# Performance work log

Measured on AMD Instinct MI355X. Metric: run time of the kernel, lower is better.

## Reference

```python
import jax, jax.numpy as jnp
import numpy as np

B, S, D = 4, 4096, 1024  # batch, seq_len, input_dim == key_dim == value_dim == output_dim


def setup_inputs() -> dict:
    key = jax.random.key(0)
    kx, kq, kk, kv, kp = jax.random.split(key, 5)
    scale = 1.0 / np.sqrt(D)
    return {
        "x": jax.random.normal(kx, (B, S, D), dtype=jnp.float32),
        # weights stored as (in_dim, out_dim) so projection is x @ W
        "Wq": jax.random.normal(kq, (D, D), dtype=jnp.float32) * scale,
        "Wk": jax.random.normal(kk, (D, D), dtype=jnp.float32) * scale,
        "Wv": jax.random.normal(kv, (D, D), dtype=jnp.float32) * scale,
        "P": jax.random.normal(kp, (D, D), dtype=jnp.float32) * scale,
    }


def reference(x, Wq, Wk, Wv, P):
    # Linear (softmax-free) self-attention, faithful to the torch module:
    # Q K^T then (.)V, materializing the (B,S,S) score matrix as the original does.
    Q = jnp.einsum("bsd,dk->bsk", x, Wq)
    K = jnp.einsum("bsd,dk->bsk", x, Wk)
    V = jnp.einsum("bsd,dv->bsv", x, Wv)
    scores = jnp.einsum("bsk,btk->bst", Q, K)   # (B,S,S)
    context = jnp.einsum("bst,btv->bsv", scores, V)
    return x + jnp.einsum("bsv,vo->bso", context, P)
```

## Files before the change

### kernel.cpp

```cpp
#include <hip/hip_runtime.h>
#include <hip/hip_bf16.h>
#include <stdint.h>


#define BATCH 4
#define SEQ   4096
#define DIM   1024

#define TRI_SLICE 589824l

typedef __bf16 bf16x8 __attribute__((ext_vector_type(8)));
typedef float f32x4 __attribute__((ext_vector_type(4)));

static __device__ __forceinline__ unsigned short f2bf(float f) {
    unsigned int u = __builtin_bit_cast(unsigned int, f);
    u += 0x7fff + ((u >> 16) & 1);
    return (unsigned short)(u >> 16);
}
static __device__ __forceinline__ float bf2f(unsigned short h) {
    unsigned int u = (unsigned int)h << 16;
    return __builtin_bit_cast(float, u);
}

__global__ __launch_bounds__(256)
void gemm_fin(const unsigned short* __restrict__ Ag,
              const unsigned short* __restrict__ Btg,
              float* __restrict__ Cg,
              int K, int lda, int ldbt, int ldc,
              long sA, long sBt, long sC)
{
    __shared__ unsigned short As[3][128][32];
    __shared__ unsigned short Bs[3][256][32];

    const int gx = gridDim.x, gy = gridDim.y;
    const int nwg = gx * gy * gridDim.z;
    int id = blockIdx.x + gx * (blockIdx.y + gy * blockIdx.z);
    id = (id & 7) * (nwg >> 3) + (id >> 3);

    const int bx = id % gx;
    const int rest = id / gx;
    const int by = rest % gy;
    const int b = rest / gy;
    const long i0 = (long)by * 128;
    const long j0 = (long)bx * 256;

    const unsigned short* A  = Ag  + (long)b * sA;
    const unsigned short* Bt = Btg + (long)b * sBt;

    const int tid  = threadIdx.x;
    const int lane = tid & 63;
    const int w    = tid >> 6;
    const int wr   = w >> 1, wc = w & 1;
    const int srow = lane >> 2;
    const int sch  = lane & 3;
    const int fr   = lane & 15;
    const int kg   = lane >> 4;
    const int ch   = (kg ^ ((fr >> 1) & 3)) * 8;

    f32x4 acc[4][8] = {};
    const int nt = K / 32;

    auto stage = [&](int t, int buf) {
        const long kk = (long)t * 32;
        const long scoff = (long)((sch ^ ((srow >> 1) & 3)) * 8);
#pragma unroll
        for (int inst = 0; inst < 2; ++inst) {
            const int row = inst * 64 + w * 16 + srow;
            const unsigned short* src = A + (i0 + row) * lda + kk + scoff;
            __builtin_amdgcn_global_load_lds(
                (const __attribute__((address_space(1))) void*)src,
                (__attribute__((address_space(3))) void*)&As[buf][inst * 64 + w * 16][0],
                16, 0, 0);
        }
#pragma unroll
        for (int inst = 0; inst < 4; ++inst) {
            const int row = inst * 64 + w * 16 + srow;
            const unsigned short* src = Bt + (j0 + row) * ldbt + kk + scoff;
            __builtin_amdgcn_global_load_lds(
                (const __attribute__((address_space(1))) void*)src,
                (__attribute__((address_space(3))) void*)&Bs[buf][inst * 64 + w * 16][0],
                16, 0, 0);
        }
    };

    stage(0, 0);
    stage(1, 1);
    stage(2, 2);

    for (int t = 0; t < nt; ++t) {
        const int buf = t % 3;
        if (t < nt - 2)      asm volatile("s_waitcnt vmcnt(12)" ::: "memory");
        else if (t == nt - 2) asm volatile("s_waitcnt vmcnt(6)" ::: "memory");
        else                 asm volatile("s_waitcnt vmcnt(0)" ::: "memory");
        __builtin_amdgcn_s_barrier();
        asm volatile("" ::: "memory");

        bf16x8 af[4], bfv[8];
#pragma unroll
        for (int m = 0; m < 4; ++m)
            af[m] = *(const bf16x8*)&As[buf][wr * 64 + m * 16 + fr][ch];
#pragma unroll
        for (int n = 0; n < 8; ++n)
            bfv[n] = *(const bf16x8*)&Bs[buf][wc * 128 + n * 16 + fr][ch];

        asm volatile("s_waitcnt lgkmcnt(0)" ::: "memory");
        __builtin_amdgcn_sched_barrier(0);
        __builtin_amdgcn_s_barrier();
        asm volatile("" ::: "memory");

        if (t + 3 < nt) stage(t + 3, buf);
        __builtin_amdgcn_sched_barrier(0);

        __builtin_amdgcn_s_setprio(1);
#pragma unroll
        for (int m = 0; m < 4; ++m)
#pragma unroll
            for (int n = 0; n < 8; ++n)
                acc[m][n] = __builtin_amdgcn_mfma_f32_16x16x32_bf16(
                    af[m], bfv[n], acc[m][n], 0, 0, 0);
        __builtin_amdgcn_s_setprio(0);
    }

    float* C32 = Cg + (long)b * sC;
#pragma unroll
    for (int m = 0; m < 4; ++m) {
        const long rbase = i0 + wr * 64 + m * 16 + kg * 4;
#pragma unroll
        for (int n = 0; n < 8; ++n) {
            const long col = j0 + wc * 128 + n * 16 + fr;
#pragma unroll
            for (int q = 0; q < 4; ++q)
                C32[(rbase + q) * ldc + col] = acc[m][n][q];
        }
    }
}

template<int OUTMODE, int BN, bool TRI, bool ADD_I>
__global__ __launch_bounds__(256)
void gemm_db(const unsigned short* __restrict__ Ag,
             const unsigned short* __restrict__ Btg,
             void* __restrict__ Cg,
             int K, int zdiv, int lda, int ldbt, int ldc,
             long sA, long sBt, long sC)
{
    constexpr int NF = BN / 32;
    __shared__ unsigned short As[2][128][64];
    __shared__ unsigned short Bs[2][BN][64];

    const int gx = gridDim.x, gy = gridDim.y;
    const int nwg = gx * gy * gridDim.z;
    int id = blockIdx.x + gx * (blockIdx.y + gy * blockIdx.z);
    id = (id & 7) * (nwg >> 3) + (id >> 3);

    int z, tlin = 0;
    long i0, j0;
    if (TRI) {
        z = id / 36;
        tlin = id % 36;
        int t = tlin, ti = 0;
        while (t > ti) { t -= ti + 1; ++ti; }
        i0 = (long)ti * 128;
        j0 = (long)t * 128;
    } else {
        const int bx = id % gx;
        const int rest = id / gx;
        const int by = rest % gy;
        z = rest / gy;
        i0 = (long)by * 128;
        j0 = (long)bx * BN;
    }
    const int b = z / zdiv;
    const long koff = (long)(z % zdiv) * K;

    const unsigned short* A  = Ag  + (long)b * sA  + koff;
    const unsigned short* Bt = Btg + (long)b * sBt + koff;

    const int tid  = threadIdx.x;
    const int lane = tid & 63;
    const int w    = tid >> 6;
    const int wr   = w >> 1, wc = w & 1;
    const int lrow = lane >> 3;
    const int lcol = lane & 7;
    const int fr   = lane & 15;
    const int kg   = lane >> 4;
    const int scol = (lcol ^ lrow) * 8;

    f32x4 acc[4][NF] = {};

    const int nt = K / 64;

    auto stage = [&](int t, int buf) {
        const long kk = (long)t * 64;
#pragma unroll
        for (int inst = 0; inst < 4; ++inst) {
            const int row = w * 32 + inst * 8;
            const unsigned short* srcA = A + (i0 + row + lrow) * lda + kk + scol;
            __builtin_amdgcn_global_load_lds(
                (const __attribute__((address_space(1))) void*)srcA,
                (__attribute__((address_space(3))) void*)&As[buf][row][0], 16, 0, 0);
        }
#pragma unroll
        for (int inst = 0; inst < NF; ++inst) {
            const int row = w * (8 * NF) + inst * 8;
            const unsigned short* srcB = Bt + (j0 + row + lrow) * ldbt + kk + scol;
            __builtin_amdgcn_global_load_lds(
                (const __attribute__((address_space(1))) void*)srcB,
                (__attribute__((address_space(3))) void*)&Bs[buf][row][0], 16, 0, 0);
        }
    };

    stage(0, 0);
    stage(1, 1);

    for (int t = 0; t < nt; ++t) {
        const int buf = t & 1;
        if (t < nt - 1) {
            if constexpr (BN == 128)
                asm volatile("s_waitcnt vmcnt(8)" ::: "memory");
            else
                asm volatile("s_waitcnt vmcnt(6)" ::: "memory");
        } else {
            asm volatile("s_waitcnt vmcnt(0)" ::: "memory");
        }
        __builtin_amdgcn_s_barrier();
        asm volatile("" ::: "memory");

        bf16x8 af0[4], bf0[NF], af1[4], bf1[NF];
        const int ch0 = (kg ^ (fr & 7)) * 8;
        const int ch1 = ((4 + kg) ^ (fr & 7)) * 8;
#pragma unroll
        for (int m = 0; m < 4; ++m)
            af0[m] = *(const bf16x8*)&As[buf][wr * 64 + m * 16 + fr][ch0];
#pragma unroll
        for (int n = 0; n < NF; ++n)
            bf0[n] = *(const bf16x8*)&Bs[buf][wc * (BN / 2) + n * 16 + fr][ch0];
#pragma unroll
        for (int m = 0; m < 4; ++m)
            af1[m] = *(const bf16x8*)&As[buf][wr * 64 + m * 16 + fr][ch1];
#pragma unroll
        for (int n = 0; n < NF; ++n)
            bf1[n] = *(const bf16x8*)&Bs[buf][wc * (BN / 2) + n * 16 + fr][ch1];

        __builtin_amdgcn_s_setprio(1);
#pragma unroll
        for (int m = 0; m < 4; ++m)
#pragma unroll
            for (int n = 0; n < NF; ++n)
                acc[m][n] = __builtin_amdgcn_mfma_f32_16x16x32_bf16(
                    af0[m], bf0[n], acc[m][n], 0, 0, 0);
        __builtin_amdgcn_s_setprio(0);

        asm volatile("s_waitcnt lgkmcnt(0)" ::: "memory");
        __builtin_amdgcn_sched_barrier(0);
        __builtin_amdgcn_s_barrier();
        asm volatile("" ::: "memory");

        if (t + 2 < nt) stage(t + 2, buf);
        __builtin_amdgcn_sched_barrier(0);

        __builtin_amdgcn_s_setprio(1);
#pragma unroll
        for (int m = 0; m < 4; ++m)
#pragma unroll
            for (int n = 0; n < NF; ++n)
                acc[m][n] = __builtin_amdgcn_mfma_f32_16x16x32_bf16(
                    af1[m], bf1[n], acc[m][n], 0, 0, 0);
        __builtin_amdgcn_s_setprio(0);
    }

    if (OUTMODE == 3) {
        unsigned short* Cp = (unsigned short*)Cg + (long)z * TRI_SLICE
                           + (long)tlin * 16384;
#pragma unroll
        for (int m = 0; m < 4; ++m) {
            const int lrb = wr * 64 + m * 16 + kg * 4;
#pragma unroll
            for (int n = 0; n < NF; ++n) {
                const int lc = wc * (BN / 2) + n * 16 + fr;
#pragma unroll
                for (int q = 0; q < 4; ++q)
                    Cp[(lrb + q) * 128 + lc] = f2bf(acc[m][n][q]);
            }
        }
        return;
    }

    unsigned short* C16 = (OUTMODE == 1) ? ((unsigned short*)Cg + (long)b * sC) : nullptr;
    float*          C32 = (OUTMODE == 0) ? ((float*)Cg + (long)b * sC)
                        : (OUTMODE == 2) ? ((float*)Cg + (long)z * sC) : nullptr;
#pragma unroll
    for (int m = 0; m < 4; ++m) {
        const long rbase = i0 + wr * 64 + m * 16 + kg * 4;
#pragma unroll
        for (int n = 0; n < NF; ++n) {
            const long col = j0 + wc * (BN / 2) + n * 16 + fr;
#pragma unroll
            for (int q = 0; q < 4; ++q) {
                const long r = rbase + q;
                float v = acc[m][n][q];
                if (ADD_I && r == col) v += 1.0f;
                if (OUTMODE == 1) C16[r * ldc + col] = f2bf(v);
                else              C32[r * ldc + col] = v;
            }
        }
    }
}

__global__ __launch_bounds__(256)
void reduce_cast_tri(const unsigned short* __restrict__ part,
                     unsigned short* __restrict__ outG, int split)
{
    const long DD = (long)DIM * DIM;
    int id = blockIdx.x * 256 + threadIdx.x;
    const int b  = id / 147456;
    int rem      = id % 147456;
    const int tlin = rem / 4096;
    const int rr = rem % 4096;
    const int r  = rr >> 5;
    const int c4 = rr & 31;
    int t = tlin, ti = 0;
    while (t > ti) { t -= ti + 1; ++ti; }
    const long off = (long)tlin * 16384 + r * 128 + c4 * 4;

    float4 s = make_float4(0.f, 0.f, 0.f, 0.f);
    for (int sp = 0; sp < split; ++sp) {
        ushort4 v = *(const ushort4*)&part[(long)(b * split + sp) * TRI_SLICE + off];
        s.x += bf2f(v.x); s.y += bf2f(v.y); s.z += bf2f(v.z); s.w += bf2f(v.w);
    }
    ushort4 o;
    o.x = f2bf(s.x); o.y = f2bf(s.y); o.z = f2bf(s.z); o.w = f2bf(s.w);
    *(ushort4*)&outG[b * DD + ((long)ti * 128 + r) * DIM + (long)t * 128 + c4 * 4] = o;
}

__global__ __launch_bounds__(256)
void reduce_cast_lin(const float* __restrict__ part, unsigned short* __restrict__ out,
                     int split, long len4)
{
    long i = (long)blockIdx.x * 256 + threadIdx.x;
    const long slab = i / len4;
    const long r = i % len4;
    float4 s = make_float4(0.f, 0.f, 0.f, 0.f);
    for (int sp = 0; sp < split; ++sp) {
        float4 v = ((const float4*)part)[(slab * split + sp) * len4 + r];
        s.x += v.x; s.y += v.y; s.z += v.z; s.w += v.w;
    }
    ushort4 o;
    o.x = f2bf(s.x); o.y = f2bf(s.y); o.z = f2bf(s.z); o.w = f2bf(s.w);
    ((ushort4*)out)[i] = o;
}

__global__ __launch_bounds__(256)
void sym_mirror(unsigned short* __restrict__ G)
{
    __shared__ unsigned short t[32][36];
    const long DD = (long)DIM * DIM;
    unsigned short* Gb = G + (long)blockIdx.z * DD;

    int u = blockIdx.y;
    int tj = 1;
    while (u >= tj) { u -= tj; ++tj; }
    const int ti = u;

    const int sr = blockIdx.x >> 2;
    const int sc = blockIdx.x & 3;
    const int row = threadIdx.x >> 3;
    const int cid = threadIdx.x & 7;

    const long srow = (long)tj * 128 + sr * 32 + row;
    const long scol = (long)ti * 128 + sc * 32 + cid * 4;
    ushort4 v = *(const ushort4*)&Gb[srow * DIM + scol];
    t[row][cid * 4 + 0] = v.x; t[row][cid * 4 + 1] = v.y;
    t[row][cid * 4 + 2] = v.z; t[row][cid * 4 + 3] = v.w;
    __syncthreads();

    const long drow = (long)ti * 128 + sc * 32 + row;
    const long dcol = (long)tj * 128 + sr * 32 + cid * 4;
    ushort4 o;
    o.x = t[cid * 4 + 0][row];
    o.y = t[cid * 4 + 1][row];
    o.z = t[cid * 4 + 2][row];
    o.w = t[cid * 4 + 3][row];
    *(ushort4*)&Gb[drow * DIM + dcol] = o;
}

__global__ __launch_bounds__(256)
void prep_all(const float* __restrict__ x,
              const float* __restrict__ Wq, const float* __restrict__ Wk,
              const float* __restrict__ Wv, const float* __restrict__ P,
              unsigned short* __restrict__ xb, unsigned short* __restrict__ xTb,
              unsigned short* __restrict__ Wqb, unsigned short* __restrict__ Wkb,
              unsigned short* __restrict__ Wvb, unsigned short* __restrict__ Ptb)
{
    __shared__ unsigned short t[32][33];
    const int z = blockIdx.z;
    const int row = threadIdx.x >> 3;
    const int cid = threadIdx.x & 7;

    if (z < BATCH) {
        const long base = (long)z * SEQ * DIM;
        const int r0 = blockIdx.y * 32;
        const int c0 = blockIdx.x * 32;
        float4 v = *(const float4*)&x[base + (long)(r0 + row) * DIM + c0 + cid * 4];
        ushort4 h;
        h.x = f2bf(v.x); h.y = f2bf(v.y); h.z = f2bf(v.z); h.w = f2bf(v.w);
        *(ushort4*)&xb[base + (long)(r0 + row) * DIM + c0 + cid * 4] = h;
        t[row][cid * 4 + 0] = h.x; t[row][cid * 4 + 1] = h.y;
        t[row][cid * 4 + 2] = h.z; t[row][cid * 4 + 3] = h.w;
        __syncthreads();
        ushort4 o;
        o.x = t[cid * 4 + 0][row];
        o.y = t[cid * 4 + 1][row];
        o.z = t[cid * 4 + 2][row];
        o.w = t[cid * 4 + 3][row];
        *(ushort4*)&xTb[base + (long)(c0 + row) * SEQ + r0 + cid * 4] = o;
        return;
    }

    const int wsel = blockIdx.y >> 5;
    const int r0 = (blockIdx.y & 31) * 32;
    const int c0 = blockIdx.x * 32;
    const float* src = (wsel == 0) ? Wq : (wsel == 1) ? Wk : (wsel == 2) ? Wv : P;
    float4 v = *(const float4*)&src[(long)(r0 + row) * DIM + c0 + cid * 4];
    ushort4 h;
    h.x = f2bf(v.x); h.y = f2bf(v.y); h.z = f2bf(v.z); h.w = f2bf(v.w);

    if (wsel < 3) {
        unsigned short* dst = (wsel == 0) ? Wqb : (wsel == 1) ? Wkb : Wvb;
        *(ushort4*)&dst[(long)(r0 + row) * DIM + c0 + cid * 4] = h;
        return;
    }
    t[row][cid * 4 + 0] = h.x; t[row][cid * 4 + 1] = h.y;
    t[row][cid * 4 + 2] = h.z; t[row][cid * 4 + 3] = h.w;
    __syncthreads();
    ushort4 o;
    o.x = t[cid * 4 + 0][row];
    o.y = t[cid * 4 + 1][row];
    o.z = t[cid * 4 + 2][row];
    o.w = t[cid * 4 + 3][row];
    *(ushort4*)&Ptb[(long)(c0 + row) * DIM + r0 + cid * 4] = o;
}

extern "C" void kernel_launch(void* const* d_in, const int* in_sizes, int n_in,
                              void* d_out, int out_size, void* d_ws, size_t ws_size,
                              hipStream_t stream)
{
    const float* x  = (const float*)d_in[0];
    const float* Wq = (const float*)d_in[1];
    const float* Wk = (const float*)d_in[2];
    const float* Wv = (const float*)d_in[3];
    const float* P  = (const float*)d_in[4];
    float* out = (float*)d_out;

    const long DD = (long)DIM * DIM;
    const long SD = (long)SEQ * DIM;

    uint8_t* ws = (uint8_t*)d_ws;
    unsigned short* xb   = (unsigned short*)(ws);
    unsigned short* xTb  = (unsigned short*)(ws + (32ul << 20));
    unsigned short* Hb   = (unsigned short*)(ws + (32ul << 20));
    unsigned short* Ntb  = (unsigned short*)(ws + (40ul << 20));
    float*          regB = (float*)(ws + (48ul << 20));
    unsigned short* Gb   = (unsigned short*)(ws + (64ul << 20));
    unsigned short* Wqb  = (unsigned short*)(ws + (72ul << 20));
    unsigned short* Ptb  = (unsigned short*)(ws + (74ul << 20));
    unsigned short* Wkb  = (unsigned short*)(ws + (76ul << 20));
    unsigned short* Wvb  = (unsigned short*)(ws + (78ul << 20));
    unsigned short* Ub   = (unsigned short*)(ws + (80ul << 20));
    unsigned short* W2Tb = (unsigned short*)(ws + (82ul << 20));
    unsigned short* regA = (unsigned short*)(ws + (84ul << 20));

    const int split = 8;

    prep_all<<<dim3(DIM / 32, SEQ / 32, BATCH + 1), 256, 0, stream>>>(
        x, Wq, Wk, Wv, P, xb, xTb, Wqb, Wkb, Wvb, Ptb);

    gemm_db<3, 128, true, false><<<dim3(36 * split * BATCH, 1, 1), 256, 0, stream>>>(
        xTb, xTb, regA, SEQ / split, split, SEQ, SEQ, DIM, SD, SD, 0);
    reduce_cast_tri<<<dim3(BATCH * 36 * 128 * 32 / 256), 256, 0, stream>>>(
        regA, Gb, split);
    sym_mirror<<<dim3(16, 28, BATCH), 256, 0, stream>>>(Gb);

    gemm_db<2, 64, false, false><<<dim3(16, 8, 4), 256, 0, stream>>>(
        Wqb, Wkb, regB, DIM / 2, 2, DIM, DIM, DIM, DD, DD, DD);
    reduce_cast_lin<<<dim3((int)(2 * DD / 4 / 256)), 256, 0, stream>>>(
        regB, Ub, 2, DD / 4);

    gemm_db<1, 64, false, false><<<dim3(16, 8, BATCH), 256, 0, stream>>>(
        Ub, Gb, Hb, DIM, 1, DIM, DIM, DIM, 0, DD, DD);

    gemm_db<1, 64, false, true><<<dim3(16, 8, BATCH), 256, 0, stream>>>(
        W2Tb, Hb, Ntb, DIM, 1, DIM, DIM, DIM, 0, DD, DD);

    gemm_fin<<<dim3(DIM / 256, SEQ / 128, BATCH), 256, 0, stream>>>(
        xb, Ntb, out, DIM, DIM, DIM, DIM, SD, DD, SD);
}
```

Baseline: 166.1 us.

## Fuse symmetric mirror into triangle reduce and drop split-K for weight GEMM

The triangle reduction kernel now also writes the transposed copy of each off-diagonal 128x128 tile through a small shared-memory transpose, so the separate sym_mirror launch and its re-read of G go away. The Wq/Wk product GEMM no longer uses split-K with an fp32 partial buffer and a reduce_cast_lin pass. It writes bf16 output directly with z=2, which removes a launch and a partial write and read. The trade-off is fewer blocks for that GEMM, so less parallelism, and a more complex reduce kernel whose shared-memory transpose may have bank conflicts.

```diff
diff --git a/kernel.cpp b/kernel.cpp
--- a/kernel.cpp
+++ b/kernel.cpp
@@ -89,9 +89,9 @@
 
     for (int t = 0; t < nt; ++t) {
         const int buf = t % 3;
-        if (t < nt - 2)      asm volatile("s_waitcnt vmcnt(12)" ::: "memory");
+        if (t < nt - 2)       asm volatile("s_waitcnt vmcnt(12)" ::: "memory");
         else if (t == nt - 2) asm volatile("s_waitcnt vmcnt(6)" ::: "memory");
-        else                 asm volatile("s_waitcnt vmcnt(0)" ::: "memory");
+        else                  asm volatile("s_waitcnt vmcnt(0)" ::: "memory");
         __builtin_amdgcn_s_barrier();
         asm volatile("" ::: "memory");
 
@@ -286,8 +286,7 @@
     }
 
     unsigned short* C16 = (OUTMODE == 1) ? ((unsigned short*)Cg + (long)b * sC) : nullptr;
-    float*          C32 = (OUTMODE == 0) ? ((float*)Cg + (long)b * sC)
-                        : (OUTMODE == 2) ? ((float*)Cg + (long)z * sC) : nullptr;
+    float*          C32 = (OUTMODE == 0) ? ((float*)Cg + (long)b * sC) : nullptr;
 #pragma unroll
     for (int m = 0; m < 4; ++m) {
         const long rbase = i0 + wr * 64 + m * 16 + kg * 4;
@@ -310,6 +309,7 @@
 void reduce_cast_tri(const unsigned short* __restrict__ part,
                      unsigned short* __restrict__ outG, int split)
 {
+    __shared__ unsigned short s[8][132];
     const long DD = (long)DIM * DIM;
     int id = blockIdx.x * 256 + threadIdx.x;
     const int b  = id / 147456;
@@ -322,65 +322,30 @@
     while (t > ti) { t -= ti + 1; ++ti; }
     const long off = (long)tlin * 16384 + r * 128 + c4 * 4;
 
-    float4 s = make_float4(0.f, 0.f, 0.f, 0.f);
+    float4 sum = make_float4(0.f, 0.f, 0.f, 0.f);
     for (int sp = 0; sp < split; ++sp) {
         ushort4 v = *(const ushort4*)&part[(long)(b * split + sp) * TRI_SLICE + off];
-        s.x += bf2f(v.x); s.y += bf2f(v.y); s.z += bf2f(v.z); s.w += bf2f(v.w);
+        sum.x += bf2f(v.x); sum.y += bf2f(v.y); sum.z += bf2f(v.z); sum.w += bf2f(v.w);
     }
     ushort4 o;
-    o.x = f2bf(s.x); o.y = f2bf(s.y); o.z = f2bf(s.z); o.w = f2bf(s.w);
+    o.x = f2bf(sum.x); o.y = f2bf(sum.y); o.z = f2bf(sum.z); o.w = f2bf(sum.w);
     *(ushort4*)&outG[b * DD + ((long)ti * 128 + r) * DIM + (long)t * 128 + c4 * 4] = o;
-}
-
-__global__ __launch_bounds__(256)
-void reduce_cast_lin(const float* __restrict__ part, unsigned short* __restrict__ out,
-                     int split, long len4)
-{
-    long i = (long)blockIdx.x * 256 + threadIdx.x;
-    const long slab = i / len4;
-    const long r = i % len4;
-    float4 s = make_float4(0.f, 0.f, 0.f, 0.f);
-    for (int sp = 0; sp < split; ++sp) {
-        float4 v = ((const float4*)part)[(slab * split + sp) * len4 + r];
-        s.x += v.x; s.y += v.y; s.z += v.z; s.w += v.w;
-    }
-    ushort4 o;
-    o.x = f2bf(s.x); o.y = f2bf(s.y); o.z = f2bf(s.z); o.w = f2bf(s.w);
-    ((ushort4*)out)[i] = o;
-}
-
-__global__ __launch_bounds__(256)
-void sym_mirror(unsigned short* __restrict__ G)
-{
-    __shared__ unsigned short t[32][36];
-    const long DD = (long)DIM * DIM;
-    unsigned short* Gb = G + (long)blockIdx.z * DD;
-
-    int u = blockIdx.y;
-    int tj = 1;
-    while (u >= tj) { u -= tj; ++tj; }
-    const int ti = u;
-
-    const int sr = blockIdx.x >> 2;
-    const int sc = blockIdx.x & 3;
-    const int row = threadIdx.x >> 3;
-    const int cid = threadIdx.x & 7;
-
-    const long srow = (long)tj * 128 + sr * 32 + row;
-    const long scol = (long)ti * 128 + sc * 32 + cid * 4;
-    ushort4 v = *(const ushort4*)&Gb[srow * DIM + scol];
-    t[row][cid * 4 + 0] = v.x; t[row][cid * 4 + 1] = v.y;
-    t[row][cid * 4 + 2] = v.z; t[row][cid * 4 + 3] = v.w;
+
+    if (t == ti) return;
+
+    const int rl = r & 7;
+    s[rl][c4 * 4 + 0] = o.x; s[rl][c4 * 4 + 1] = o.y;
+    s[rl][c4 * 4 + 2] = o.z; s[rl][c4 * 4 + 3] = o.w;
     __syncthreads();
 
-    const long drow = (long)ti * 128 + sc * 32 + row;
-    const long dcol = (long)tj * 128 + sr * 32 + cid * 4;
-    ushort4 o;
-    o.x = t[cid * 4 + 0][row];
-    o.y = t[cid * 4 + 1][row];
-    o.z = t[cid * 4 + 2][row];
-    o.w = t[cid * 4 + 3][row];
-    *(ushort4*)&Gb[drow * DIM + dcol] = o;
+    const int r0 = r & ~7;
+    const int co = threadIdx.x >> 1;
+    const int hf = threadIdx.x & 1;
+    ushort4 m;
+    m.x = s[hf * 4 + 0][co]; m.y = s[hf * 4 + 1][co];
+    m.z = s[hf * 4 + 2][co]; m.w = s[hf * 4 + 3][co];
+    *(ushort4*)&outG[b * DD + ((long)t * 128 + co) * DIM
+                     + (long)ti * 128 + r0 + hf * 4] = m;
 }
 
 __global__ __launch_bounds__(256)
@@ -459,7 +424,6 @@
     unsigned short* xTb  = (unsigned short*)(ws + (32ul << 20));
     unsigned short* Hb   = (unsigned short*)(ws + (32ul << 20));
     unsigned short* Ntb  = (unsigned short*)(ws + (40ul << 20));
-    float*          regB = (float*)(ws + (48ul << 20));
     unsigned short* Gb   = (unsigned short*)(ws + (64ul << 20));
     unsigned short* Wqb  = (unsigned short*)(ws + (72ul << 20));
     unsigned short* Ptb  = (unsigned short*)(ws + (74ul << 20));
@@ -478,12 +442,9 @@
         xTb, xTb, regA, SEQ / split, split, SEQ, SEQ, DIM, SD, SD, 0);
     reduce_cast_tri<<<dim3(BATCH * 36 * 128 * 32 / 256), 256, 0, stream>>>(
         regA, Gb, split);
-    sym_mirror<<<dim3(16, 28, BATCH), 256, 0, stream>>>(Gb);
-
-    gemm_db<2, 64, false, false><<<dim3(16, 8, 4), 256, 0, stream>>>(
-        Wqb, Wkb, regB, DIM / 2, 2, DIM, DIM, DIM, DD, DD, DD);
-    reduce_cast_lin<<<dim3((int)(2 * DD / 4 / 256)), 256, 0, stream>>>(
-        regB, Ub, 2, DD / 4);
+
+    gemm_db<1, 64, false, false><<<dim3(16, 8, 2), 256, 0, stream>>>(
+        Wqb, Wkb, Ub, DIM, 1, DIM, DIM, DIM, DD, DD, DD);
 
     gemm_db<1, 64, false, false><<<dim3(16, 8, BATCH), 256, 0, stream>>>(
         Ub, Gb, Hb, DIM, 1, DIM, DIM, DIM, 0, DD, DD);
```

New measurement: 165.0 us. No clear change (-0.7%).
